# Optimization experiments

Measured on AMD Instinct MI355X. Metric: run time of the kernel, lower is better.

## Reference

```python
import jax, jax.numpy as jnp
import numpy as np

N_ROW = 512
N_COL = 512
N_RAY = 131072   # ~256 views x 512 detector channels
N_INT = 768      # padded max grid-line intersections per ray


def setup_inputs() -> dict:
    key = jax.random.key(0)
    k1, k2, k3, k4 = jax.random.split(key, 4)
    image = jax.random.normal(k1, (N_ROW, N_COL), dtype=jnp.float32)
    # sorted ray parameters in [0, 1] (fractions along src->dst)
    t_sorted = jnp.sort(jax.random.uniform(k2, (N_RAY, N_INT), dtype=jnp.float32), axis=-1)
    M = jnp.eye(2, dtype=jnp.float32)          # pixel spacing = 1
    b = jnp.zeros((2,), dtype=jnp.float32)     # image origin at (0, 0)
    # fan-beam-like geometry: sources on a circle around image center
    center = jnp.array([255.5, 255.5], dtype=jnp.float32)
    radius = 400.0
    ang = jax.random.uniform(k3, (N_RAY,), dtype=jnp.float32, minval=0.0, maxval=2.0 * np.pi)
    off = jax.random.uniform(k4, (N_RAY,), dtype=jnp.float32, minval=-0.3, maxval=0.3)
    src = center + radius * jnp.stack([jnp.cos(ang), jnp.sin(ang)], axis=-1)
    dst = center - radius * jnp.stack([jnp.cos(ang + off), jnp.sin(ang + off)], axis=-1)
    return {"image": image, "t_sorted": t_sorted, "M": M, "b": b, "src": src, "dst": dst}


def reference(image, t_sorted, M, b, src, dst):
    n_row, n_col = image.shape
    M_inv = jnp.linalg.inv(M)
    # intersection points along each ray: [n_ray, n_int, 2]
    pts = src[:, None, :] + t_sorted[:, :, None] * (dst - src)[:, None, :]
    x0, y0 = pts[:, :-1, 0], pts[:, :-1, 1]
    x1, y1 = pts[:, 1:, 0], pts[:, 1:, 1]
    inf_mask = jnp.isinf(x0) | jnp.isinf(x1) | jnp.isinf(y0) | jnp.isinf(y1)
    seg_len = jnp.sqrt((x1 - x0) ** 2 + (y1 - y0) ** 2)
    # segment midpoints -> pixel indices via inverse affine transform
    mx = 0.5 * (x0 + x1) - b[0]
    my = 0.5 * (y0 + y1) - b[1]
    rowf = M_inv[0, 0] * mx + M_inv[0, 1] * my
    colf = M_inv[1, 0] * mx + M_inv[1, 1] * my
    row_idx = jnp.round(rowf).astype(jnp.int32)
    col_idx = jnp.round(colf).astype(jnp.int32)
    oob = (row_idx < 0) | (row_idx >= n_row) | (col_idx < 0) | (col_idx >= n_col)
    valid = (~inf_mask) & (~oob)
    flat_idx = jnp.where(valid, row_idx * n_col + col_idx, 0)
    pixel_vals = image.reshape(-1)[flat_idx]          # gather [n_ray, n_int-1]
    segment_val = jnp.where(valid, pixel_vals * seg_len, 0.0)
    return segment_val.sum(axis=1)                    # sinogram [n_ray]
```

## Files before the change

### kernel.cpp

```cpp
#include <hip/hip_runtime.h>

#define N_ROW 512
#define N_COL 512
#define N_INT 768
#define N_SEG (N_INT - 1)
#define WAVES_PER_BLOCK 4

__global__ __launch_bounds__(WAVES_PER_BLOCK * 64)
void ct_fwd_kernel(const float* __restrict__ image,
                   const float* __restrict__ t_sorted,
                   const float* __restrict__ M,
                   const float* __restrict__ b,
                   const float* __restrict__ src,
                   const float* __restrict__ dst,
                   float* __restrict__ out,
                   int n_ray)
{
#pragma clang fp contract(off)
    const int wave = threadIdx.x >> 6;
    const int lane = threadIdx.x & 63;
    const int ray  = blockIdx.x * WAVES_PER_BLOCK + wave;
    if (ray >= n_ray) return;

    const float m00 = M[0], m01 = M[1], m10 = M[2], m11 = M[3];
    const float det  = m00 * m11 - m01 * m10;
    const float rdet = 1.0f / det;
    const float i00 =  m11 * rdet;
    const float i01 = -(m01 * rdet);
    const float i10 = -(m10 * rdet);
    const float i11 =  m00 * rdet;
    const float b0 = b[0], b1 = b[1];

    const float sx  = src[2 * ray];
    const float sy  = src[2 * ray + 1];
    const float ddx = dst[2 * ray]     - sx;
    const float ddy = dst[2 * ray + 1] - sy;

    const float* __restrict__ tp = t_sorted + (size_t)ray * N_INT;

    float acc = 0.0f;
#pragma unroll
    for (int k = 0; k < (N_INT + 63) / 64; ++k) {
        const int j = k * 64 + lane;
        if (j < N_SEG) {
            const float t0 = tp[j];
            const float t1 = tp[j + 1];

            const float px0 = t0 * ddx;
            const float py0 = t0 * ddy;
            const float px1 = t1 * ddx;
            const float py1 = t1 * ddy;
            const float x0 = sx + px0;
            const float y0 = sy + py0;
            const float x1 = sx + px1;
            const float y1 = sy + py1;

            const float ex = x1 - x0;
            const float ey = y1 - y0;
            const float ex2 = ex * ex;
            const float ey2 = ey * ey;
            const float seg = __fsqrt_rn(ex2 + ey2);

            const float sxm = x0 + x1;
            const float sym = y0 + y1;
            const float mx = 0.5f * sxm - b0;
            const float my = 0.5f * sym - b1;

            const float r0 = i00 * mx;
            const float r1 = i01 * my;
            const float c0 = i10 * mx;
            const float c1 = i11 * my;
            const float rowf = r0 + r1;
            const float colf = c0 + c1;

            const int ri = (int)rintf(rowf);
            const int ci = (int)rintf(colf);

            const bool valid = (ri >= 0) & (ri < N_ROW) & (ci >= 0) & (ci < N_COL);
            const int flat = valid ? (ri * N_COL + ci) : 0;
            const float pv = image[flat];
            acc += valid ? pv * seg : 0.0f;
        }
    }

#pragma unroll
    for (int off = 32; off > 0; off >>= 1)
        acc += __shfl_down(acc, off, 64);

    if (lane == 0) out[ray] = acc;
}

extern "C" void kernel_launch(void* const* d_in, const int* in_sizes, int n_in,
                              void* d_out, int out_size, void* d_ws, size_t ws_size,
                              hipStream_t stream)
{
    const float* image    = (const float*)d_in[0];
    const float* t_sorted = (const float*)d_in[1];
    const float* M        = (const float*)d_in[2];
    const float* b        = (const float*)d_in[3];
    const float* src      = (const float*)d_in[4];
    const float* dst      = (const float*)d_in[5];
    float* out = (float*)d_out;

    const int n_ray = in_sizes[4] / 2;
    const int grid = (n_ray + WAVES_PER_BLOCK - 1) / WAVES_PER_BLOCK;
    ct_fwd_kernel<<<grid, WAVES_PER_BLOCK * 64, 0, stream>>>(
        image, t_sorted, M, b, src, dst, out, n_ray);
}
```

Measured before the change: 726.2 us.

## Load ray parameters as float4 and share segment endpoints via wave shuffles

Each lane now loads three float4 chunks of the ray's t values instead of two overlapping scalar loads per segment. Each intersection point is computed once. The right endpoint of a lane's last segment in each chunk comes from a shuffle from the neighbouring lane, with lane 0 of the next chunk feeding lane 63. This cuts global load instructions and duplicated point arithmetic. In exchange it adds cross-lane shuffles and changes the per-lane summation order.

```diff
diff --git a/kernel.cpp b/kernel.cpp
--- a/kernel.cpp
+++ b/kernel.cpp
@@ -4,9 +4,9 @@
 #define N_COL 512
 #define N_INT 768
 #define N_SEG (N_INT - 1)
-#define WAVES_PER_BLOCK 4
+#define WPB 4
 
-__global__ __launch_bounds__(WAVES_PER_BLOCK * 64)
+__global__ __launch_bounds__(WPB * 64)
 void ct_fwd_kernel(const float* __restrict__ image,
                    const float* __restrict__ t_sorted,
                    const float* __restrict__ M,
@@ -19,7 +19,7 @@
 #pragma clang fp contract(off)
     const int wave = threadIdx.x >> 6;
     const int lane = threadIdx.x & 63;
-    const int ray  = blockIdx.x * WAVES_PER_BLOCK + wave;
+    const int ray  = blockIdx.x * WPB + wave;
     if (ray >= n_ray) return;
 
     const float m00 = M[0], m01 = M[1], m10 = M[2], m11 = M[3];
@@ -36,24 +36,41 @@
     const float ddx = dst[2 * ray]     - sx;
     const float ddy = dst[2 * ray + 1] - sy;
 
-    const float* __restrict__ tp = t_sorted + (size_t)ray * N_INT;
+    const float4* __restrict__ tp4 =
+        (const float4*)(t_sorted + (size_t)ray * N_INT);
+    const float4 q0 = tp4[lane];
+    const float4 q1 = tp4[64 + lane];
+    const float4 q2 = tp4[128 + lane];
+
+    const float tv[12] = {q0.x, q0.y, q0.z, q0.w,
+                          q1.x, q1.y, q1.z, q1.w,
+                          q2.x, q2.y, q2.z, q2.w};
+    float X[12], Y[12];
+#pragma unroll
+    for (int i = 0; i < 12; ++i) {
+        const float px = tv[i] * ddx;
+        const float py = tv[i] * ddy;
+        X[i] = sx + px;
+        Y[i] = sy + py;
+    }
 
     float acc = 0.0f;
 #pragma unroll
-    for (int k = 0; k < (N_INT + 63) / 64; ++k) {
-        const int j = k * 64 + lane;
-        if (j < N_SEG) {
-            const float t0 = tp[j];
-            const float t1 = tp[j + 1];
-
-            const float px0 = t0 * ddx;
-            const float py0 = t0 * ddy;
-            const float px1 = t1 * ddx;
-            const float py1 = t1 * ddy;
-            const float x0 = sx + px0;
-            const float y0 = sy + py0;
-            const float x1 = sx + px1;
-            const float y1 = sy + py1;
+    for (int c = 0; c < 3; ++c) {
+        float nX = __shfl_down(X[4 * c], 1, 64);
+        float nY = __shfl_down(Y[4 * c], 1, 64);
+        if (c < 2) {
+            const float bX = __shfl(X[4 * c + 4], 0, 64);
+            const float bY = __shfl(Y[4 * c + 4], 0, 64);
+            if (lane == 63) { nX = bX; nY = bY; }
+        }
+#pragma unroll
+        for (int i = 0; i < 4; ++i) {
+            const float x0 = X[4 * c + i];
+            const float y0 = Y[4 * c + i];
+            const float x1 = (i < 3) ? X[4 * c + i + 1] : nX;
+            const float y1 = (i < 3) ? Y[4 * c + i + 1] : nY;
+            const bool segv = !((c == 2) & (i == 3) & (lane == 63));
 
             const float ex = x1 - x0;
             const float ey = y1 - y0;
@@ -76,7 +93,8 @@
             const int ri = (int)rintf(rowf);
             const int ci = (int)rintf(colf);
 
-            const bool valid = (ri >= 0) & (ri < N_ROW) & (ci >= 0) & (ci < N_COL);
+            const bool valid = (ri >= 0) & (ri < N_ROW) &
+                               (ci >= 0) & (ci < N_COL) & segv;
             const int flat = valid ? (ri * N_COL + ci) : 0;
             const float pv = image[flat];
             acc += valid ? pv * seg : 0.0f;
@@ -103,7 +121,7 @@
     float* out = (float*)d_out;
 
     const int n_ray = in_sizes[4] / 2;
-    const int grid = (n_ray + WAVES_PER_BLOCK - 1) / WAVES_PER_BLOCK;
-    ct_fwd_kernel<<<grid, WAVES_PER_BLOCK * 64, 0, stream>>>(
+    const int grid = (n_ray + WPB - 1) / WPB;
+    ct_fwd_kernel<<<grid, WPB * 64, 0, stream>>>(
         image, t_sorted, M, b, src, dst, out, n_ray);
 }
```

Measured after the change: 635.3 us. 1.14x faster.
